# Kernel optimization log

Hardware: AMD Instinct MI355X
Metric: run time of the kernel (lower is better)

## Reference

```python
import jax, jax.numpy as jnp
import numpy as np

B, S = 128, 128
AH, VH, TH = 64, 64, 128  # audio/vision/text LSTM hidden sizes
FUSED = (AH + 1) * (VH + 1) * (TH + 1)  # 545025
PF = 128  # post_fusion_dim


def setup_inputs() -> dict:
    key = jax.random.key(0)
    ks = jax.random.split(key, 6)
    return {
        "audio_h": jax.random.normal(ks[0], (B, S, AH), jnp.float32),
        "vision_h": jax.random.normal(ks[1], (B, S, VH), jnp.float32),
        "text_h": jax.random.normal(ks[2], (B, S, TH), jnp.float32),
        "W1": jax.random.normal(ks[3], (PF, FUSED), jnp.float32) * 0.001,
        "b1": jnp.zeros((PF,), jnp.float32),
        "W2": jax.random.normal(ks[4], (PF, PF), jnp.float32) * 0.05,
        "b2": jnp.zeros((PF,), jnp.float32),
        "W3": jax.random.normal(ks[5], (1, PF), jnp.float32) * 0.05,
        "b3": jnp.zeros((1,), jnp.float32),
    }


def reference(audio_h, vision_h, text_h, W1, b1, W2, b2, W3, b3):
    b, s = audio_h.shape[0], audio_h.shape[1]
    ones = jnp.ones((b, s, 1), audio_h.dtype)
    a = jnp.concatenate([ones, audio_h], axis=2)   # [B,S,AH+1]
    v = jnp.concatenate([ones, vision_h], axis=2)  # [B,S,VH+1]
    t = jnp.concatenate([ones, text_h], axis=2)    # [B,S,TH+1]
    # sum_t outer(a_t, v_t, t_t): one fused contraction over the time axis
    fusion = jnp.einsum('bsa,bsv,bsw->bavw', a, v, t)  # [B,AH+1,VH+1,TH+1]
    fusion = fusion.reshape(b, -1)                      # matches torch view order (a,v,t)
    # T2FN low-rank regularizer scale
    tmp = jnp.sqrt(jnp.asarray(AH * VH * TH / max(AH, VH, TH), jnp.float32))
    # post-fusion MLP (dropout p=0 -> identity)
    y1 = jax.nn.relu(fusion @ W1.T + b1)
    y2 = jax.nn.relu(y1 @ W2.T + b2)
    out = y2 @ W3.T + b3  # [B,1]
    out = jax.nn.sigmoid(out) * 6.0 - 3.0  # output_range=6, output_shift=-3
    norm = jnp.linalg.norm(fusion, axis=1)  # [B]
    reg_loss = jnp.mean(tmp * norm)
    return (out, reg_loss)
```

## Files before the change

### kernel.cpp

```cpp
#include <hip/hip_runtime.h>
#include <math.h>

#define BB 128
#define SS 128
#define AE 65
#define VE 65
#define TE 129
#define PFD 128
#define FUSED 545025UL
#define FUSEDI 545025
#define VSTRIDE 136
#define APLANE 8840
#define FPP 574976UL
#define FPPI 574976
#define KSP 512
#define NBLK 1123

typedef _Float16 half8 __attribute__((ext_vector_type(8)));
typedef float f32x16 __attribute__((ext_vector_type(16)));

__device__ __forceinline__ void gll16(const void* g, void* l) {
  __builtin_amdgcn_global_load_lds((const __attribute__((address_space(1))) void*)g,
                                   (__attribute__((address_space(3))) void*)l, 16, 0, 0);
}

__global__ __launch_bounds__(256) void k_zero(float* __restrict__ p, int n) {
  int i = blockIdx.x * 256 + threadIdx.x;
  if (i < n) p[i] = 0.f;
}

__global__ __launch_bounds__(256) void k_fpad(_Float16* __restrict__ Fh) {
  const int b = blockIdx.x;
  _Float16* base = Fh + (size_t)b * FPP;
  for (int i = threadIdx.x; i < 29575; i += 256) {
    const int a = i / 455, r = i - a * 455;
    const int v = r / 7, e = r - v * 7;
    base[a * APLANE + v * VSTRIDE + 129 + e] = (_Float16)0.f;
  }
  for (int i = threadIdx.x; i < 376; i += 256) base[574600 + i] = (_Float16)0.f;
}

__global__ __launch_bounds__(256) void k_core(
    const float* __restrict__ audio, const float* __restrict__ vision,
    const float* __restrict__ text, _Float16* __restrict__ Fh,
    float* __restrict__ normsq)
{
  const int b  = blockIdx.x;
  const int gy = blockIdx.y;
  const int gz = blockIdx.z;
  const int tid = threadIdx.x;
  const int wv = tid >> 6, ln = tid & 63;
  const int lr = ln & 31, hb = ln >> 5;

  __shared__ float    sVt[64][132];
  __shared__ float    sAc[8][132];
  __shared__ _Float16 sTh[64][136];
  __shared__ _Float16 sTl[64][136];

  {
    const float* vb = vision + (size_t)b * SS * 64;
#pragma unroll
    for (int r = 0; r < 32; ++r) {
      const int e = tid + 256 * r;
      sVt[e & 63][e >> 6] = vb[e];
    }
    const float* ab = audio + (size_t)b * SS * 64 + 8 * gy;
#pragma unroll
    for (int r = 0; r < 4; ++r) {
      const int e = tid + 256 * r;
      sAc[e & 7][e >> 3] = ab[(e >> 3) * 64 + (e & 7)];
    }
    const int wbase = 64 * gz;
    const float* tb = text + (size_t)b * SS * 128;
#pragma unroll
    for (int r = 0; r < 32; ++r) {
      const int e = tid + 256 * r;
      const int s = e >> 6, wl = e & 63;
      const int w = wbase + wl;
      const float val = (w == 0) ? 1.f : tb[s * 128 + w - 1];
      const _Float16 th = (_Float16)val;
      sTh[wl][s] = th;
      sTl[wl][s] = (_Float16)((val - (float)th) * 2048.f);
    }
  }
  __syncthreads();

  float ss = 0.f;
  for (int i = 0; i < 8; ++i) {
    const int u  = 8 * wv + i;
    const int rt = u >> 1, wt = u & 1;
    const int j  = rt >> 1, vh = rt & 1;
    const int v0m = 32 * vh;
    const int wl0 = 32 * wt;

    f32x16 acc = {}, accl = {};
#pragma unroll
    for (int ks = 0; ks < 8; ++ks) {
      const int s0 = 16 * ks + 8 * hb;
      const float4 x0 = *(const float4*)&sVt[v0m + lr][s0];
      const float4 x1 = *(const float4*)&sVt[v0m + lr][s0 + 4];
      const float4 a0 = *(const float4*)&sAc[j][s0];
      const float4 a1 = *(const float4*)&sAc[j][s0 + 4];
      const float pp[8] = {a0.x * x0.x, a0.y * x0.y, a0.z * x0.z, a0.w * x0.w,
                           a1.x * x1.x, a1.y * x1.y, a1.z * x1.z, a1.w * x1.w};
      half8 afh, afl;
#pragma unroll
      for (int e = 0; e < 8; ++e) {
        const _Float16 h = (_Float16)pp[e];
        afh[e] = h;
        afl[e] = (_Float16)((pp[e] - (float)h) * 2048.f);
      }
      const half8 bqh = *(const half8*)&sTh[wl0 + lr][s0];
      const half8 bql = *(const half8*)&sTl[wl0 + lr][s0];
      acc  = __builtin_amdgcn_mfma_f32_32x32x16_f16(afh, bqh, acc,  0, 0, 0);
      accl = __builtin_amdgcn_mfma_f32_32x32x16_f16(afl, bqh, accl, 0, 0, 0);
      accl = __builtin_amdgcn_mfma_f32_32x32x16_f16(afh, bql, accl, 0, 0, 0);
    }

    const int a = 1 + 8 * gy + j;
    _Float16* Fb = Fh + (size_t)b * FPP + (size_t)a * APLANE;
    const int wg = 64 * gz + wl0 + lr;
#pragma unroll
    for (int reg = 0; reg < 16; ++reg) {
      const int crow = (reg & 3) + 8 * (reg >> 2) + 4 * hb;
      const int v = 1 + 32 * vh + crow;
      const float f = acc[reg] + accl[reg] * (1.f / 2048.f);
      ss += f * f;
      Fb[(size_t)v * VSTRIDE + wg] = (_Float16)f;
    }
  }

#pragma unroll
  for (int off = 32; off > 0; off >>= 1) ss += __shfl_down(ss, off);
  if (ln == 0) atomicAdd(&normsq[b], ss);
}

__global__ __launch_bounds__(256) void k_pa(
    const float* __restrict__ vision, const float* __restrict__ text,
    _Float16* __restrict__ Fh, float* __restrict__ normsq)
{
  const int b = blockIdx.x;
  const int tid = threadIdx.x;
  const int tw = tid & 15, tv = tid >> 4;
  __shared__ float sv[32][80];
  __shared__ float st[32][144];
  float acc[5][9];
#pragma unroll
  for (int i = 0; i < 5; ++i)
#pragma unroll
    for (int j = 0; j < 9; ++j) acc[i][j] = 0.f;

  for (int c = 0; c < 4; ++c) {
    const int s0 = 32 * c;
    __syncthreads();
    const float* vbase = &vision[((size_t)(b * SS + s0)) * 64];
#pragma unroll
    for (int r = 0; r < 8; ++r) {
      const int e = tid + 256 * r;
      sv[e >> 6][(e & 63) + 1] = vbase[e];
    }
    const float* tbase = &text[((size_t)(b * SS + s0)) * 128];
#pragma unroll
    for (int r = 0; r < 16; ++r) {
      const int e = tid + 256 * r;
      st[e >> 7][(e & 127) + 1] = tbase[e];
    }
    if (tid < 32) { sv[tid][0] = 1.f; st[tid][0] = 1.f; }
    __syncthreads();
    for (int s = 0; s < 32; ++s) {
      float vr[5], tr[9];
#pragma unroll
      for (int i = 0; i < 5; ++i) {
        const int vx = tv + 16 * i;
        vr[i] = (vx < VE) ? sv[s][vx] : 0.f;
      }
#pragma unroll
      for (int j = 0; j < 9; ++j) {
        const int wx = tw + 16 * j;
        tr[j] = (wx < TE) ? st[s][wx] : 0.f;
      }
#pragma unroll
      for (int i = 0; i < 5; ++i)
#pragma unroll
        for (int j = 0; j < 9; ++j) acc[i][j] += vr[i] * tr[j];
    }
  }
  _Float16* Fb = Fh + (size_t)b * FPP;
  float ss = 0.f;
#pragma unroll
  for (int i = 0; i < 5; ++i) {
    const int v = tv + 16 * i;
    if (v < VE) {
#pragma unroll
      for (int j = 0; j < 9; ++j) {
        const int w = tw + 16 * j;
        if (w < TE) {
          const float m = acc[i][j];
          Fb[(size_t)v * VSTRIDE + w] = (_Float16)m;
          ss += m * m;
        }
      }
    }
  }
#pragma unroll
  for (int off = 32; off > 0; off >>= 1) ss += __shfl_down(ss, off);
  if ((tid & 63) == 0) atomicAdd(&normsq[b], ss);
}

__global__ __launch_bounds__(256) void k_pv(
    const float* __restrict__ audio, const float* __restrict__ text,
    _Float16* __restrict__ Fh, float* __restrict__ normsq)
{
  const int b = blockIdx.x;
  const int tid = threadIdx.x;
  const int tw = tid & 15, tv = tid >> 4;
  __shared__ float sa[32][64];
  __shared__ float st[32][144];
  float acc[4][9];
#pragma unroll
  for (int i = 0; i < 4; ++i)
#pragma unroll
    for (int j = 0; j < 9; ++j) acc[i][j] = 0.f;

  for (int c = 0; c < 4; ++c) {
    const int s0 = 32 * c;
    __syncthreads();
    const float* abase = &audio[((size_t)(b * SS + s0)) * 64];
#pragma unroll
    for (int r = 0; r < 8; ++r) {
      const int e = tid + 256 * r;
      sa[e >> 6][e & 63] = abase[e];
    }
    const float* tbase = &text[((size_t)(b * SS + s0)) * 128];
#pragma unroll
    for (int r = 0; r < 16; ++r) {
      const int e = tid + 256 * r;
      st[e >> 7][(e & 127) + 1] = tbase[e];
    }
    if (tid < 32) st[tid][0] = 1.f;
    __syncthreads();
    for (int s = 0; s < 32; ++s) {
      float ar[4], tr[9];
#pragma unroll
      for (int i = 0; i < 4; ++i) ar[i] = sa[s][tv + 16 * i];
#pragma unroll
      for (int j = 0; j < 9; ++j) {
        const int wx = tw + 16 * j;
        tr[j] = (wx < TE) ? st[s][wx] : 0.f;
      }
#pragma unroll
      for (int i = 0; i < 4; ++i)
#pragma unroll
        for (int j = 0; j < 9; ++j) acc[i][j] += ar[i] * tr[j];
    }
  }
  float ss = 0.f;
#pragma unroll
  for (int i = 0; i < 4; ++i) {
    const int a = 1 + tv + 16 * i;
    _Float16* Fb = Fh + (size_t)b * FPP + (size_t)a * APLANE;
#pragma unroll
    for (int j = 0; j < 9; ++j) {
      const int w = tw + 16 * j;
      if (w < TE) {
        const float m = acc[i][j];
        Fb[w] = (_Float16)m;
        ss += m * m;
      }
    }
  }
#pragma unroll
  for (int off = 32; off > 0; off >>= 1) ss += __shfl_down(ss, off);
  if ((tid & 63) == 0) atomicAdd(&normsq[b], ss);
}

__global__ __launch_bounds__(256) void k_wlast(
    const float* __restrict__ audio, const float* __restrict__ vision,
    const float* __restrict__ text, _Float16* __restrict__ Fh,
    float* __restrict__ Flast, float* __restrict__ normsq)
{
  const int b = blockIdx.x;
  const int tid = threadIdx.x;
  const int tw = tid & 15, tv = tid >> 4;
  __shared__ float sa[32][64];
  __shared__ float sv[32][64];
  __shared__ float swt[32];
  float acc[4][4];
#pragma unroll
  for (int i = 0; i < 4; ++i)
#pragma unroll
    for (int j = 0; j < 4; ++j) acc[i][j] = 0.f;

  for (int c = 0; c < 4; ++c) {
    const int s0 = 32 * c;
    __syncthreads();
    const float* abase = &audio[((size_t)(b * SS + s0)) * 64];
    const float* vbase = &vision[((size_t)(b * SS + s0)) * 64];
#pragma unroll
    for (int r = 0; r < 8; ++r) {
      const int e = tid + 256 * r;
      sa[e >> 6][e & 63] = abase[e];
      sv[e >> 6][e & 63] = vbase[e];
    }
    if (tid < 32) swt[tid] = text[((size_t)(b * SS + s0 + tid)) * 128 + 127];
    __syncthreads();
    for (int s = 0; s < 32; ++s) {
      const float t = swt[s];
      float ar[4], vr[4];
#pragma unroll
      for (int i = 0; i < 4; ++i) ar[i] = sa[s][tv + 16 * i] * t;
#pragma unroll
      for (int j = 0; j < 4; ++j) vr[j] = sv[s][tw + 16 * j];
#pragma unroll
      for (int i = 0; i < 4; ++i)
#pragma unroll
        for (int j = 0; j < 4; ++j) acc[i][j] += ar[i] * vr[j];
    }
  }
  float ss = 0.f;
#pragma unroll
  for (int i = 0; i < 4; ++i) {
    const int a = 1 + tv + 16 * i;
    _Float16* Fb = Fh + (size_t)b * FPP + (size_t)a * APLANE;
#pragma unroll
    for (int j = 0; j < 4; ++j) {
      const int v = 1 + tw + 16 * j;
      float m = acc[i][j];
      ss += m * m;
      if (a == 64 && v == 64) { Flast[b] = m; m = 0.f; }
      Fb[(size_t)v * VSTRIDE + 128] = (_Float16)m;
    }
  }
#pragma unroll
  for (int off = 32; off > 0; off >>= 1) ss += __shfl_down(ss, off);
  if ((tid & 63) == 0) atomicAdd(&normsq[b], ss);
}

__global__ __launch_bounds__(256) void k_gemm(
    const float* __restrict__ W1, const _Float16* __restrict__ Fh,
    float* __restrict__ parts)
{
  __shared__ _Float16 sB[3][4096];

  const int tid = threadIdx.x;
  const int wv = tid >> 6, ln = tid & 63;
  const int lb = ln & 31, hb = ln >> 5;
  const int p  = (wv << 5) + lb;
  const int kp0 = blockIdx.x * KSP;
  const int kpl0 = kp0 + (hb << 3);
  const int kpl1 = kpl0 + 16;

  int w0, ko0, w1, ko1;
  {
    const int a0 = kpl0 / APLANE; const int r0 = kpl0 - a0 * APLANE;
    const int v0 = r0 / VSTRIDE;  w0 = r0 - v0 * VSTRIDE;
    ko0 = a0 * 8385 + v0 * 129 + w0;
    const int a1 = kpl1 / APLANE; const int r1 = kpl1 - a1 * APLANE;
    const int v1 = r1 / VSTRIDE;  w1 = r1 - v1 * VSTRIDE;
    ko1 = a1 * 8385 + v1 * 129 + w1;
  }

  const float* wrow = W1 + (size_t)p * FUSED;

  const int brow0 = (wv << 5) + (ln >> 2);
  const int slogB = (ln & 3) ^ ((ln >> 2) & 3);
  const _Float16* FhP0 = Fh + (size_t)brow0 * FPP + kp0 + (slogB << 3);
  const _Float16* FhP1 = FhP0 + (size_t)16 * FPP;

  f32x16 acc0 = {}, acc1 = {}, acc2 = {}, acc3 = {};
  float4 xa[4];

#define LOADA                                                              \
  {                                                                        \
    const int kc0 = (ko0 <= 545017) ? ko0 : 545008;                        \
    const int kc1 = (ko1 <= 545017) ? ko1 : 545008;                        \
    __builtin_memcpy(&xa[0], wrow + kc0, 16);                              \
    __builtin_memcpy(&xa[1], wrow + kc0 + 4, 16);                          \
    __builtin_memcpy(&xa[2], wrow + kc1, 16);                              \
    __builtin_memcpy(&xa[3], wrow + kc1 + 4, 16);                          \
    w0 += 32; if (w0 >= VSTRIDE) { w0 -= VSTRIDE; ko0 += 25; } else ko0 += 32; \
    w1 += 32; if (w1 >= VSTRIDE) { w1 -= VSTRIDE; ko1 += 25; } else ko1 += 32; \
  }

#define STAGEB(BUF, KOFF)                                                 \
  {                                                                       \
    gll16(FhP0 + (KOFF), (char*)&sB[BUF][0] + ((wv << 5) << 6));          \
    gll16(FhP1 + (KOFF), (char*)&sB[BUF][0] + (((wv << 5) + 16) << 6));   \
  }

#define GSTEP(T, WSTR)                                                         \
  {                                                                            \
    asm volatile("s_waitcnt " WSTR ::: "memory");                              \
    __builtin_amdgcn_sched_barrier(0);                                         \
    __builtin_amdgcn_s_barrier();                                              \
    __builtin_amdgcn_sched_barrier(0);                                         \
    half8 af0, af1;                                                            \
    af0[0] = (_Float16)xa[0].x; af0[1] = (_Float16)xa[0].y;                    \
    af0[2] = (_Float16)xa[0].z; af0[3] = (_Float16)xa[0].w;                    \
    af0[4] = (_Float16)xa[1].x; af0[5] = (_Float16)xa[1].y;                    \
    af0[6] = (_Float16)xa[1].z; af0[7] = (_Float16)xa[1].w;                    \
    af1[0] = (_Float16)xa[2].x; af1[1] = (_Float16)xa[2].y;                    \
    af1[2] = (_Float16)xa[2].z; af1[3] = (_Float16)xa[2].w;                    \
    af1[4] = (_Float16)xa[3].x; af1[5] = (_Float16)xa[3].y;                    \
    af1[6] = (_Float16)xa[3].z; af1[7] = (_Float16)xa[3].w;                    \
    if ((T) + 1 < 16) { LOADA }                                                \
    if ((T) + 2 < 16) { STAGEB(((T) + 2) % 3, ((T) + 2) * 32) }                \
    __builtin_amdgcn_sched_barrier(0);                                         \
    {                                                                          \
      const _Float16* sBb = &sB[(T) % 3][0];                                   \
      {                                                                        \
        const int sl = hb;                                                     \
        const char* bbase = (const char*)sBb + (lb << 6) + ((sl ^ (lb & 3)) << 4); \
        const half8 b0 = *(const half8*)(bbase);                               \
        const half8 b1 = *(const half8*)(bbase + 2048);                        \
        const half8 b2 = *(const half8*)(bbase + 4096);                        \
        const half8 b3 = *(const half8*)(bbase + 6144);                        \
        acc0 = __builtin_amdgcn_mfma_f32_32x32x16_f16(af0, b0, acc0, 0, 0, 0); \
        acc1 = __builtin_amdgcn_mfma_f32_32x32x16_f16(af0, b1, acc1, 0, 0, 0); \
        acc2 = __builtin_amdgcn_mfma_f32_32x32x16_f16(af0, b2, acc2, 0, 0, 0); \
        acc3 = __builtin_amdgcn_mfma_f32_32x32x16_f16(af0, b3, acc3, 0, 0, 0); \
      }                                                                        \
      {                                                                        \
        const int sl = 2 + hb;                                                 \
        const char* bbase = (const char*)sBb + (lb << 6) + ((sl ^ (lb & 3)) << 4); \
        const half8 b0 = *(const half8*)(bbase);                               \
        const half8 b1 = *(const half8*)(bbase + 2048);                        \
        const half8 b2 = *(const half8*)(bbase + 4096);                        \
        const half8 b3 = *(const half8*)(bbase + 6144);                        \
        acc0 = __builtin_amdgcn_mfma_f32_32x32x16_f16(af1, b0, acc0, 0, 0, 0); \
        acc1 = __builtin_amdgcn_mfma_f32_32x32x16_f16(af1, b1, acc1, 0, 0, 0); \
        acc2 = __builtin_amdgcn_mfma_f32_32x32x16_f16(af1, b2, acc2, 0, 0, 0); \
        acc3 = __builtin_amdgcn_mfma_f32_32x32x16_f16(af1, b3, acc3, 0, 0, 0); \
      }                                                                        \
    }                                                                          \
  }

  LOADA
  STAGEB(0, 0)
  STAGEB(1, 32)

  GSTEP(0,  "vmcnt(2)")
  GSTEP(1,  "vmcnt(2)")
  GSTEP(2,  "vmcnt(2)")
  GSTEP(3,  "vmcnt(2)")
  GSTEP(4,  "vmcnt(2)")
  GSTEP(5,  "vmcnt(2)")
  GSTEP(6,  "vmcnt(2)")
  GSTEP(7,  "vmcnt(2)")
  GSTEP(8,  "vmcnt(2)")
  GSTEP(9,  "vmcnt(2)")
  GSTEP(10, "vmcnt(2)")
  GSTEP(11, "vmcnt(2)")
  GSTEP(12, "vmcnt(2)")
  GSTEP(13, "vmcnt(2)")
  GSTEP(14, "vmcnt(2)")
  GSTEP(15, "vmcnt(0)")
#undef GSTEP
#undef LOADA
#undef STAGEB

  f32x16* o = (f32x16*)(parts + ((size_t)blockIdx.x * 256 + tid) * 64);
  o[0] = acc0; o[1] = acc1; o[2] = acc2; o[3] = acc3;
}

__global__ __launch_bounds__(256) void k_red(const float* __restrict__ parts,
                                             float* __restrict__ y1pre)
{
  const int tid = threadIdx.x;
  const int T = blockIdx.x * 4 + (tid >> 6);
  const int R = tid & 63;
  float s = 0.f;
  for (int sl = blockIdx.y; sl < NBLK; sl += 16)
    s += parts[(size_t)sl * 16384 + T * 64 + R];
  const int wv2 = T >> 6, hb2 = (T >> 5) & 1, lb2 = T & 31;
  const int q = R >> 4, rg = R & 15;
  const int b = q * 32 + lb2;
  const int pp = wv2 * 32 + (rg & 3) + 8 * (rg >> 2) + 4 * hb2;
  atomicAdd(&y1pre[b * PFD + pp], s);
}

__global__ __launch_bounds__(128) void k_final(
    const float* __restrict__ y1pre, const float* __restrict__ b1,
    const float* __restrict__ W2, const float* __restrict__ b2,
    const float* __restrict__ W3, const float* __restrict__ b3,
    const float* __restrict__ W1, const float* __restrict__ Flast,
    float* __restrict__ out)
{
  const int b = blockIdx.x, p = threadIdx.x;
  __shared__ float y1[PFD];
  __shared__ float red[PFD];
  const float extra = W1[(size_t)p * FUSED + (FUSED - 1)] * Flast[b];
  y1[p] = fmaxf(y1pre[(size_t)b * PFD + p] + extra + b1[p], 0.f);
  __syncthreads();
  float s = b2[p];
  for (int k = 0; k < PFD; ++k) s += y1[k] * W2[p * PFD + k];
  const float y2 = fmaxf(s, 0.f);
  red[p] = y2 * W3[p];
  __syncthreads();
  for (int off = 64; off > 0; off >>= 1) {
    if (p < off) red[p] += red[p + off];
    __syncthreads();
  }
  if (p == 0) {
    const float x = red[0] + b3[0];
    out[b] = 6.f / (1.f + expf(-x)) - 3.f;
  }
}

__global__ __launch_bounds__(128) void k_reg(const float* __restrict__ normsq,
                                             float* __restrict__ out)
{
  const int t = threadIdx.x;
  __shared__ float red[BB];
  red[t] = sqrtf(normsq[t]);
  __syncthreads();
  for (int off = 64; off > 0; off >>= 1) {
    if (t < off) red[t] += red[t + off];
    __syncthreads();
  }
  if (t == 0) out[BB] = 64.f * red[0] / (float)BB;
}

extern "C" void kernel_launch(void* const* d_in, const int* in_sizes, int n_in,
                              void* d_out, int out_size, void* d_ws, size_t ws_size,
                              hipStream_t stream) {
  const float* audio  = (const float*)d_in[0];
  const float* vision = (const float*)d_in[1];
  const float* text   = (const float*)d_in[2];
  const float* W1     = (const float*)d_in[3];
  const float* b1     = (const float*)d_in[4];
  const float* W2     = (const float*)d_in[5];
  const float* b2     = (const float*)d_in[6];
  const float* W3     = (const float*)d_in[7];
  const float* b3     = (const float*)d_in[8];
  float* out = (float*)d_out;

  float* y1pre  = (float*)d_ws;
  float* normsq = y1pre + BB * PFD;
  float* Flast  = normsq + BB;
  _Float16* Fh  = (_Float16*)((char*)d_ws + 131072);
  float* parts  = (float*)((char*)d_ws + 147324928);

  k_zero<<<65, 256, 0, stream>>>(y1pre, BB * PFD + 2 * BB);
  k_fpad<<<BB, 256, 0, stream>>>(Fh);

  k_core<<<dim3(BB, 8, 2), 256, 0, stream>>>(audio, vision, text, Fh, normsq);
  k_pa<<<BB, 256, 0, stream>>>(vision, text, Fh, normsq);
  k_pv<<<BB, 256, 0, stream>>>(audio, text, Fh, normsq);
  k_wlast<<<BB, 256, 0, stream>>>(audio, vision, text, Fh, Flast, normsq);

  k_gemm<<<NBLK, 256, 0, stream>>>(W1, Fh, parts);
  k_red<<<dim3(64, 16), 256, 0, stream>>>(parts, y1pre);

  k_final<<<BB, PFD, 0, stream>>>(y1pre, b1, W2, b2, W3, b3, W1, Flast, out);
  k_reg<<<1, BB, 0, stream>>>(normsq, out);
}
```

Baseline: 382.3 us.

## Merge small kernels into fewer launches and double-buffer W1 register prefetch

Folds the zero-init and padding kernels into one, merges the three plane-computing kernels into a single launch with a blockIdx.y selector, and folds the regularizer reduction into the final MLP kernel. This cuts launch count and lets small per-batch kernels run concurrently. Separately, the GEMM now keeps two register buffers of W1 rows so that global loads for the A operand are issued two steps ahead, with the wait count relaxed to match. The deeper prefetch raises register pressure, which may reduce occupancy in the GEMM.

Result: faster. 335.3 us (-12.3%).

```diff
diff --git a/kernel.cpp b/kernel.cpp
--- a/kernel.cpp
+++ b/kernel.cpp
@@ -24,20 +24,22 @@
                                    (__attribute__((address_space(3))) void*)l, 16, 0, 0);
 }
 
-__global__ __launch_bounds__(256) void k_zero(float* __restrict__ p, int n) {
-  int i = blockIdx.x * 256 + threadIdx.x;
-  if (i < n) p[i] = 0.f;
-}
-
-__global__ __launch_bounds__(256) void k_fpad(_Float16* __restrict__ Fh) {
+__global__ __launch_bounds__(256) void k_initf(_Float16* __restrict__ Fh,
+                                               float* __restrict__ y1pre,
+                                               float* __restrict__ normsq,
+                                               float* __restrict__ Flast) {
   const int b = blockIdx.x;
+  const int tid = threadIdx.x;
   _Float16* base = Fh + (size_t)b * FPP;
-  for (int i = threadIdx.x; i < 29575; i += 256) {
+  for (int i = tid; i < 29575; i += 256) {
     const int a = i / 455, r = i - a * 455;
     const int v = r / 7, e = r - v * 7;
     base[a * APLANE + v * VSTRIDE + 129 + e] = (_Float16)0.f;
   }
-  for (int i = threadIdx.x; i < 376; i += 256) base[574600 + i] = (_Float16)0.f;
+  for (int i = tid; i < 376; i += 256) base[574600 + i] = (_Float16)0.f;
+  if (tid < PFD) y1pre[b * PFD + tid] = 0.f;
+  if (tid == 128) normsq[b] = 0.f;
+  if (tid == 129) Flast[b] = 0.f;
 }
 
 __global__ __launch_bounds__(256) void k_core(
@@ -135,202 +137,185 @@
   if (ln == 0) atomicAdd(&normsq[b], ss);
 }
 
-__global__ __launch_bounds__(256) void k_pa(
-    const float* __restrict__ vision, const float* __restrict__ text,
-    _Float16* __restrict__ Fh, float* __restrict__ normsq)
-{
-  const int b = blockIdx.x;
-  const int tid = threadIdx.x;
-  const int tw = tid & 15, tv = tid >> 4;
-  __shared__ float sv[32][80];
-  __shared__ float st[32][144];
-  float acc[5][9];
-#pragma unroll
-  for (int i = 0; i < 5; ++i)
-#pragma unroll
-    for (int j = 0; j < 9; ++j) acc[i][j] = 0.f;
-
-  for (int c = 0; c < 4; ++c) {
-    const int s0 = 32 * c;
-    __syncthreads();
-    const float* vbase = &vision[((size_t)(b * SS + s0)) * 64];
-#pragma unroll
-    for (int r = 0; r < 8; ++r) {
-      const int e = tid + 256 * r;
-      sv[e >> 6][(e & 63) + 1] = vbase[e];
-    }
-    const float* tbase = &text[((size_t)(b * SS + s0)) * 128];
-#pragma unroll
-    for (int r = 0; r < 16; ++r) {
-      const int e = tid + 256 * r;
-      st[e >> 7][(e & 127) + 1] = tbase[e];
-    }
-    if (tid < 32) { sv[tid][0] = 1.f; st[tid][0] = 1.f; }
-    __syncthreads();
-    for (int s = 0; s < 32; ++s) {
-      float vr[5], tr[9];
-#pragma unroll
-      for (int i = 0; i < 5; ++i) {
-        const int vx = tv + 16 * i;
-        vr[i] = (vx < VE) ? sv[s][vx] : 0.f;
-      }
-#pragma unroll
-      for (int j = 0; j < 9; ++j) {
-        const int wx = tw + 16 * j;
-        tr[j] = (wx < TE) ? st[s][wx] : 0.f;
-      }
-#pragma unroll
-      for (int i = 0; i < 5; ++i)
-#pragma unroll
-        for (int j = 0; j < 9; ++j) acc[i][j] += vr[i] * tr[j];
-    }
-  }
-  _Float16* Fb = Fh + (size_t)b * FPP;
-  float ss = 0.f;
-#pragma unroll
-  for (int i = 0; i < 5; ++i) {
-    const int v = tv + 16 * i;
-    if (v < VE) {
-#pragma unroll
-      for (int j = 0; j < 9; ++j) {
-        const int w = tw + 16 * j;
-        if (w < TE) {
-          const float m = acc[i][j];
-          Fb[(size_t)v * VSTRIDE + w] = (_Float16)m;
-          ss += m * m;
-        }
-      }
-    }
-  }
-#pragma unroll
-  for (int off = 32; off > 0; off >>= 1) ss += __shfl_down(ss, off);
-  if ((tid & 63) == 0) atomicAdd(&normsq[b], ss);
-}
-
-__global__ __launch_bounds__(256) void k_pv(
-    const float* __restrict__ audio, const float* __restrict__ text,
-    _Float16* __restrict__ Fh, float* __restrict__ normsq)
-{
-  const int b = blockIdx.x;
-  const int tid = threadIdx.x;
-  const int tw = tid & 15, tv = tid >> 4;
-  __shared__ float sa[32][64];
-  __shared__ float st[32][144];
-  float acc[4][9];
-#pragma unroll
-  for (int i = 0; i < 4; ++i)
-#pragma unroll
-    for (int j = 0; j < 9; ++j) acc[i][j] = 0.f;
-
-  for (int c = 0; c < 4; ++c) {
-    const int s0 = 32 * c;
-    __syncthreads();
-    const float* abase = &audio[((size_t)(b * SS + s0)) * 64];
-#pragma unroll
-    for (int r = 0; r < 8; ++r) {
-      const int e = tid + 256 * r;
-      sa[e >> 6][e & 63] = abase[e];
-    }
-    const float* tbase = &text[((size_t)(b * SS + s0)) * 128];
-#pragma unroll
-    for (int r = 0; r < 16; ++r) {
-      const int e = tid + 256 * r;
-      st[e >> 7][(e & 127) + 1] = tbase[e];
-    }
-    if (tid < 32) st[tid][0] = 1.f;
-    __syncthreads();
-    for (int s = 0; s < 32; ++s) {
-      float ar[4], tr[9];
-#pragma unroll
-      for (int i = 0; i < 4; ++i) ar[i] = sa[s][tv + 16 * i];
-#pragma unroll
-      for (int j = 0; j < 9; ++j) {
-        const int wx = tw + 16 * j;
-        tr[j] = (wx < TE) ? st[s][wx] : 0.f;
-      }
-#pragma unroll
-      for (int i = 0; i < 4; ++i)
-#pragma unroll
-        for (int j = 0; j < 9; ++j) acc[i][j] += ar[i] * tr[j];
-    }
-  }
-  float ss = 0.f;
-#pragma unroll
-  for (int i = 0; i < 4; ++i) {
-    const int a = 1 + tv + 16 * i;
-    _Float16* Fb = Fh + (size_t)b * FPP + (size_t)a * APLANE;
-#pragma unroll
-    for (int j = 0; j < 9; ++j) {
-      const int w = tw + 16 * j;
-      if (w < TE) {
-        const float m = acc[i][j];
-        Fb[w] = (_Float16)m;
-        ss += m * m;
-      }
-    }
-  }
-#pragma unroll
-  for (int off = 32; off > 0; off >>= 1) ss += __shfl_down(ss, off);
-  if ((tid & 63) == 0) atomicAdd(&normsq[b], ss);
-}
-
-__global__ __launch_bounds__(256) void k_wlast(
+__global__ __launch_bounds__(256) void k_planes(
     const float* __restrict__ audio, const float* __restrict__ vision,
     const float* __restrict__ text, _Float16* __restrict__ Fh,
     float* __restrict__ Flast, float* __restrict__ normsq)
 {
   const int b = blockIdx.x;
+  const int which = blockIdx.y;
   const int tid = threadIdx.x;
   const int tw = tid & 15, tv = tid >> 4;
-  __shared__ float sa[32][64];
-  __shared__ float sv[32][64];
-  __shared__ float swt[32];
-  float acc[4][4];
-#pragma unroll
-  for (int i = 0; i < 4; ++i)
-#pragma unroll
-    for (int j = 0; j < 4; ++j) acc[i][j] = 0.f;
-
-  for (int c = 0; c < 4; ++c) {
-    const int s0 = 32 * c;
-    __syncthreads();
-    const float* abase = &audio[((size_t)(b * SS + s0)) * 64];
-    const float* vbase = &vision[((size_t)(b * SS + s0)) * 64];
-#pragma unroll
-    for (int r = 0; r < 8; ++r) {
-      const int e = tid + 256 * r;
-      sa[e >> 6][e & 63] = abase[e];
-      sv[e >> 6][e & 63] = vbase[e];
-    }
-    if (tid < 32) swt[tid] = text[((size_t)(b * SS + s0 + tid)) * 128 + 127];
-    __syncthreads();
-    for (int s = 0; s < 32; ++s) {
-      const float t = swt[s];
-      float ar[4], vr[4];
-#pragma unroll
-      for (int i = 0; i < 4; ++i) ar[i] = sa[s][tv + 16 * i] * t;
-#pragma unroll
-      for (int j = 0; j < 4; ++j) vr[j] = sv[s][tw + 16 * j];
-#pragma unroll
-      for (int i = 0; i < 4; ++i)
-#pragma unroll
-        for (int j = 0; j < 4; ++j) acc[i][j] += ar[i] * vr[j];
-    }
-  }
+  __shared__ __align__(16) char smem[28800];
+
   float ss = 0.f;
-#pragma unroll
-  for (int i = 0; i < 4; ++i) {
-    const int a = 1 + tv + 16 * i;
-    _Float16* Fb = Fh + (size_t)b * FPP + (size_t)a * APLANE;
-#pragma unroll
-    for (int j = 0; j < 4; ++j) {
-      const int v = 1 + tw + 16 * j;
-      float m = acc[i][j];
-      ss += m * m;
-      if (a == 64 && v == 64) { Flast[b] = m; m = 0.f; }
-      Fb[(size_t)v * VSTRIDE + 128] = (_Float16)m;
-    }
-  }
+
+  if (which == 0) {
+    float (*sv)[80]  = (float(*)[80])smem;
+    float (*st)[144] = (float(*)[144])(smem + 10240);
+    float acc[5][9];
+#pragma unroll
+    for (int i = 0; i < 5; ++i)
+#pragma unroll
+      for (int j = 0; j < 9; ++j) acc[i][j] = 0.f;
+
+    for (int c = 0; c < 4; ++c) {
+      const int s0 = 32 * c;
+      __syncthreads();
+      const float* vbase = &vision[((size_t)(b * SS + s0)) * 64];
+#pragma unroll
+      for (int r = 0; r < 8; ++r) {
+        const int e = tid + 256 * r;
+        sv[e >> 6][(e & 63) + 1] = vbase[e];
+      }
+      const float* tbase = &text[((size_t)(b * SS + s0)) * 128];
+#pragma unroll
+      for (int r = 0; r < 16; ++r) {
+        const int e = tid + 256 * r;
+        st[e >> 7][(e & 127) + 1] = tbase[e];
+      }
+      if (tid < 32) { sv[tid][0] = 1.f; st[tid][0] = 1.f; }
+      __syncthreads();
+      for (int s = 0; s < 32; ++s) {
+        float vr[5], tr[9];
+#pragma unroll
+        for (int i = 0; i < 5; ++i) {
+          const int vx = tv + 16 * i;
+          vr[i] = (vx < VE) ? sv[s][vx] : 0.f;
+        }
+#pragma unroll
+        for (int j = 0; j < 9; ++j) {
+          const int wx = tw + 16 * j;
+          tr[j] = (wx < TE) ? st[s][wx] : 0.f;
+        }
+#pragma unroll
+        for (int i = 0; i < 5; ++i)
+#pragma unroll
+          for (int j = 0; j < 9; ++j) acc[i][j] += vr[i] * tr[j];
+      }
+    }
+    _Float16* Fb = Fh + (size_t)b * FPP;
+#pragma unroll
+    for (int i = 0; i < 5; ++i) {
+      const int v = tv + 16 * i;
+      if (v < VE) {
+#pragma unroll
+        for (int j = 0; j < 9; ++j) {
+          const int w = tw + 16 * j;
+          if (w < TE) {
+            const float m = acc[i][j];
+            Fb[(size_t)v * VSTRIDE + w] = (_Float16)m;
+            ss += m * m;
+          }
+        }
+      }
+    }
+  } else if (which == 1) {
+    float (*sa)[64]  = (float(*)[64])smem;
+    float (*st)[144] = (float(*)[144])(smem + 10240);
+    float acc[4][9];
+#pragma unroll
+    for (int i = 0; i < 4; ++i)
+#pragma unroll
+      for (int j = 0; j < 9; ++j) acc[i][j] = 0.f;
+
+    for (int c = 0; c < 4; ++c) {
+      const int s0 = 32 * c;
+      __syncthreads();
+      const float* abase = &audio[((size_t)(b * SS + s0)) * 64];
+#pragma unroll
+      for (int r = 0; r < 8; ++r) {
+        const int e = tid + 256 * r;
+        sa[e >> 6][e & 63] = abase[e];
+      }
+      const float* tbase = &text[((size_t)(b * SS + s0)) * 128];
+#pragma unroll
+      for (int r = 0; r < 16; ++r) {
+        const int e = tid + 256 * r;
+        st[e >> 7][(e & 127) + 1] = tbase[e];
+      }
+      if (tid < 32) st[tid][0] = 1.f;
+      __syncthreads();
+      for (int s = 0; s < 32; ++s) {
+        float ar[4], tr[9];
+#pragma unroll
+        for (int i = 0; i < 4; ++i) ar[i] = sa[s][tv + 16 * i];
+#pragma unroll
+        for (int j = 0; j < 9; ++j) {
+          const int wx = tw + 16 * j;
+          tr[j] = (wx < TE) ? st[s][wx] : 0.f;
+        }
+#pragma unroll
+        for (int i = 0; i < 4; ++i)
+#pragma unroll
+          for (int j = 0; j < 9; ++j) acc[i][j] += ar[i] * tr[j];
+      }
+    }
+#pragma unroll
+    for (int i = 0; i < 4; ++i) {
+      const int a = 1 + tv + 16 * i;
+      _Float16* Fb = Fh + (size_t)b * FPP + (size_t)a * APLANE;
+#pragma unroll
+      for (int j = 0; j < 9; ++j) {
+        const int w = tw + 16 * j;
+        if (w < TE) {
+          const float m = acc[i][j];
+          Fb[w] = (_Float16)m;
+          ss += m * m;
+        }
+      }
+    }
+  } else {
+    float (*sa)[64] = (float(*)[64])smem;
+    float (*sv)[64] = (float(*)[64])(smem + 10240);
+    float* swt = (float*)(smem + 10240 + 8192);
+    float acc[4][4];
+#pragma unroll
+    for (int i = 0; i < 4; ++i)
+#pragma unroll
+      for (int j = 0; j < 4; ++j) acc[i][j] = 0.f;
+
+    for (int c = 0; c < 4; ++c) {
+      const int s0 = 32 * c;
+      __syncthreads();
+      const float* abase = &audio[((size_t)(b * SS + s0)) * 64];
+      const float* vbase = &vision[((size_t)(b * SS + s0)) * 64];
+#pragma unroll
+      for (int r = 0; r < 8; ++r) {
+        const int e = tid + 256 * r;
+        sa[e >> 6][e & 63] = abase[e];
+        sv[e >> 6][e & 63] = vbase[e];
+      }
+      if (tid < 32) swt[tid] = text[((size_t)(b * SS + s0 + tid)) * 128 + 127];
+      __syncthreads();
+      for (int s = 0; s < 32; ++s) {
+        const float t = swt[s];
+        float ar[4], vr[4];
+#pragma unroll
+        for (int i = 0; i < 4; ++i) ar[i] = sa[s][tv + 16 * i] * t;
+#pragma unroll
+        for (int j = 0; j < 4; ++j) vr[j] = sv[s][tw + 16 * j];
+#pragma unroll
+        for (int i = 0; i < 4; ++i)
+#pragma unroll
+          for (int j = 0; j < 4; ++j) acc[i][j] += ar[i] * vr[j];
+      }
+    }
+#pragma unroll
+    for (int i = 0; i < 4; ++i) {
+      const int a = 1 + tv + 16 * i;
+      _Float16* Fb = Fh + (size_t)b * FPP + (size_t)a * APLANE;
+#pragma unroll
+      for (int j = 0; j < 4; ++j) {
+        const int v = 1 + tw + 16 * j;
+        float m = acc[i][j];
+        ss += m * m;
+        if (a == 64 && v == 64) { Flast[b] = m; m = 0.f; }
+        Fb[(size_t)v * VSTRIDE + 128] = (_Float16)m;
+      }
+    }
+  }
+
 #pragma unroll
   for (int off = 32; off > 0; off >>= 1) ss += __shfl_down(ss, off);
   if ((tid & 63) == 0) atomicAdd(&normsq[b], ss);
@@ -368,16 +353,16 @@
   const _Float16* FhP1 = FhP0 + (size_t)16 * FPP;
 
   f32x16 acc0 = {}, acc1 = {}, acc2 = {}, acc3 = {};
-  float4 xa[4];
-
-#define LOADA                                                              \
+  float4 xaP[4], xaQ[4];
+
+#define LOADA(S)                                                           \
   {                                                                        \
     const int kc0 = (ko0 <= 545017) ? ko0 : 545008;                        \
     const int kc1 = (ko1 <= 545017) ? ko1 : 545008;                        \
-    __builtin_memcpy(&xa[0], wrow + kc0, 16);                              \
-    __builtin_memcpy(&xa[1], wrow + kc0 + 4, 16);                          \
-    __builtin_memcpy(&xa[2], wrow + kc1, 16);                              \
-    __builtin_memcpy(&xa[3], wrow + kc1 + 4, 16);                          \
+    __builtin_memcpy(&xa##S[0], wrow + kc0, 16);                           \
+    __builtin_memcpy(&xa##S[1], wrow + kc0 + 4, 16);                       \
+    __builtin_memcpy(&xa##S[2], wrow + kc1, 16);                           \
+    __builtin_memcpy(&xa##S[3], wrow + kc1 + 4, 16);                       \
     w0 += 32; if (w0 >= VSTRIDE) { w0 -= VSTRIDE; ko0 += 25; } else ko0 += 32; \
     w1 += 32; if (w1 >= VSTRIDE) { w1 -= VSTRIDE; ko1 += 25; } else ko1 += 32; \
   }
@@ -388,23 +373,22 @@
     gll16(FhP1 + (KOFF), (char*)&sB[BUF][0] + (((wv << 5) + 16) << 6));   \
   }
 
-#define GSTEP(T, WSTR)                                                         \
+#define GSTEP(T, S, WSTR)                                                      \
   {                                                                            \
     asm volatile("s_waitcnt " WSTR ::: "memory");                              \
     __builtin_amdgcn_sched_barrier(0);                                         \
     __builtin_amdgcn_s_barrier();                                              \
     __builtin_amdgcn_sched_barrier(0);                                         \
     half8 af0, af1;                                                            \
-    af0[0] = (_Float16)xa[0].x; af0[1] = (_Float16)xa[0].y;                    \
-    af0[2] = (_Float16)xa[0].z; af0[3] = (_Float16)xa[0].w;                    \
-    af0[4] = (_Float16)xa[1].x; af0[5] = (_Float16)xa[1].y;                    \
-    af0[6] = (_Float16)xa[1].z; af0[7] = (_Float16)xa[1].w;                    \
-    af1[0] = (_Float16)xa[2].x; af1[1] = (_Float16)xa[2].y;                    \
-    af1[2] = (_Float16)xa[2].z; af1[3] = (_Float16)xa[2].w;                    \
-    af1[4] = (_Float16)xa[3].x; af1[5] = (_Float16)xa[3].y;                    \
-    af1[6] = (_Float16)xa[3].z; af1[7] = (_Float16)xa[3].w;                    \
-    if ((T) + 1 < 16) { LOADA }                                                \
-    if ((T) + 2 < 16) { STAGEB(((T) + 2) % 3, ((T) + 2) * 32) }                \
+    af0[0] = (_Float16)xa##S[0].x; af0[1] = (_Float16)xa##S[0].y;              \
+    af0[2] = (_Float16)xa##S[0].z; af0[3] = (_Float16)xa##S[0].w;              \
+    af0[4] = (_Float16)xa##S[1].x; af0[5] = (_Float16)xa##S[1].y;              \
+    af0[6] = (_Float16)xa##S[1].z; af0[7] = (_Float16)xa##S[1].w;              \
+    af1[0] = (_Float16)xa##S[2].x; af1[1] = (_Float16)xa##S[2].y;              \
+    af1[2] = (_Float16)xa##S[2].z; af1[3] = (_Float16)xa##S[2].w;              \
+    af1[4] = (_Float16)xa##S[3].x; af1[5] = (_Float16)xa##S[3].y;              \
+    af1[6] = (_Float16)xa##S[3].z; af1[7] = (_Float16)xa##S[3].w;              \
+    if ((T) + 2 < 16) { LOADA(S) STAGEB(((T) + 2) % 3, ((T) + 2) * 32) }       \
     __builtin_amdgcn_sched_barrier(0);                                         \
     {                                                                          \
       const _Float16* sBb = &sB[(T) % 3][0];                                   \
@@ -435,26 +419,27 @@
     }                                                                          \
   }
 
-  LOADA
+  LOADA(P)
   STAGEB(0, 0)
+  LOADA(Q)
   STAGEB(1, 32)
 
-  GSTEP(0,  "vmcnt(2)")
-  GSTEP(1,  "vmcnt(2)")
-  GSTEP(2,  "vmcnt(2)")
-  GSTEP(3,  "vmcnt(2)")
-  GSTEP(4,  "vmcnt(2)")
-  GSTEP(5,  "vmcnt(2)")
-  GSTEP(6,  "vmcnt(2)")
-  GSTEP(7,  "vmcnt(2)")
-  GSTEP(8,  "vmcnt(2)")
-  GSTEP(9,  "vmcnt(2)")
-  GSTEP(10, "vmcnt(2)")
-  GSTEP(11, "vmcnt(2)")
-  GSTEP(12, "vmcnt(2)")
-  GSTEP(13, "vmcnt(2)")
-  GSTEP(14, "vmcnt(2)")
-  GSTEP(15, "vmcnt(0)")
+  GSTEP(0,  P, "vmcnt(6)")
+  GSTEP(1,  Q, "vmcnt(6)")
+  GSTEP(2,  P, "vmcnt(6)")
+  GSTEP(3,  Q, "vmcnt(6)")
+  GSTEP(4,  P, "vmcnt(6)")
+  GSTEP(5,  Q, "vmcnt(6)")
+  GSTEP(6,  P, "vmcnt(6)")
+  GSTEP(7,  Q, "vmcnt(6)")
+  GSTEP(8,  P, "vmcnt(6)")
+  GSTEP(9,  Q, "vmcnt(6)")
+  GSTEP(10, P, "vmcnt(6)")
+  GSTEP(11, Q, "vmcnt(6)")
+  GSTEP(12, P, "vmcnt(6)")
+  GSTEP(13, Q, "vmcnt(6)")
+  GSTEP(14, P, "vmcnt(6)")
+  GSTEP(15, Q, "vmcnt(0)")
 #undef GSTEP
 #undef LOADA
 #undef STAGEB
@@ -484,7 +469,7 @@
     const float* __restrict__ W2, const float* __restrict__ b2,
     const float* __restrict__ W3, const float* __restrict__ b3,
     const float* __restrict__ W1, const float* __restrict__ Flast,
-    float* __restrict__ out)
+    const float* __restrict__ normsq, float* __restrict__ out)
 {
   const int b = blockIdx.x, p = threadIdx.x;
   __shared__ float y1[PFD];
@@ -505,20 +490,16 @@
     const float x = red[0] + b3[0];
     out[b] = 6.f / (1.f + expf(-x)) - 3.f;
   }
-}
-
-__global__ __launch_bounds__(128) void k_reg(const float* __restrict__ normsq,
-                                             float* __restrict__ out)
-{
-  const int t = threadIdx.x;
-  __shared__ float red[BB];
-  red[t] = sqrtf(normsq[t]);
-  __syncthreads();
-  for (int off = 64; off > 0; off >>= 1) {
-    if (t < off) red[t] += red[t + off];
+  if (b == 0) {
     __syncthreads();
-  }
-  if (t == 0) out[BB] = 64.f * red[0] / (float)BB;
+    red[p] = sqrtf(normsq[p]);
+    __syncthreads();
+    for (int off = 64; off > 0; off >>= 1) {
+      if (p < off) red[p] += red[p + off];
+      __syncthreads();
+    }
+    if (p == 0) out[BB] = 64.f * red[0] / (float)BB;
+  }
 }
 
 extern "C" void kernel_launch(void* const* d_in, const int* in_sizes, int n_in,
@@ -541,17 +522,13 @@
   _Float16* Fh  = (_Float16*)((char*)d_ws + 131072);
   float* parts  = (float*)((char*)d_ws + 147324928);
 
-  k_zero<<<65, 256, 0, stream>>>(y1pre, BB * PFD + 2 * BB);
-  k_fpad<<<BB, 256, 0, stream>>>(Fh);
+  k_initf<<<BB, 256, 0, stream>>>(Fh, y1pre, normsq, Flast);
 
   k_core<<<dim3(BB, 8, 2), 256, 0, stream>>>(audio, vision, text, Fh, normsq);
-  k_pa<<<BB, 256, 0, stream>>>(vision, text, Fh, normsq);
-  k_pv<<<BB, 256, 0, stream>>>(audio, text, Fh, normsq);
-  k_wlast<<<BB, 256, 0, stream>>>(audio, vision, text, Fh, Flast, normsq);
+  k_planes<<<dim3(BB, 3), 256, 0, stream>>>(audio, vision, text, Fh, Flast, normsq);
 
   k_gemm<<<NBLK, 256, 0, stream>>>(W1, Fh, parts);
   k_red<<<dim3(64, 16), 256, 0, stream>>>(parts, y1pre);
 
-  k_final<<<BB, PFD, 0, stream>>>(y1pre, b1, W2, b2, W3, b3, W1, Flast, out);
-  k_reg<<<1, BB, 0, stream>>>(normsq, out);
-}
+  k_final<<<BB, PFD, 0, stream>>>(y1pre, b1, W2, b2, W3, b3, W1, Flast, normsq, out);
+}
```
